# Performance work log

Hardware: AMD Instinct MI355X
Metric: run time of the kernel (lower is better)

Reference implementation:

```python
import jax, jax.numpy as jnp
import numpy as np

N, C, L, E = 10000, 128, 9, 5  # nodes, channels, (lmax+1)^2, num_elements
INV_SQRT_C = 1.0 / np.sqrt(C).astype(np.float32)


def _sparse(key, shape, p=0.15):
    # mimic the sparsity of e3nn CG coupling (U) tensors
    k1, k2 = jax.random.split(key)
    mask = jax.random.bernoulli(k1, p, shape)
    vals = jax.random.normal(k2, shape, dtype=jnp.float32)
    return jnp.where(mask, vals, 0.0)


def setup_inputs() -> dict:
    key = jax.random.key(0)
    ks = jax.random.split(key, 16)
    node_feats = jax.random.normal(ks[0], (N, C, L), dtype=jnp.float32)
    node_attrs = jax.nn.one_hot(jax.random.randint(ks[1], (N,), 0, E), E, dtype=jnp.float32)
    sc = jax.random.normal(ks[2], (N, 512), dtype=jnp.float32)
    # CG coupling tensors U_nu per output irrep (constant buffers in the torch module)
    # l_out = 0 (d=1): path counts k3=10, k2=3, k1=1
    U3_0 = _sparse(ks[3], (1, L, L, L, 10))
    U2_0 = _sparse(ks[4], (1, L, L, 3))
    U1_0 = _sparse(ks[5], (1, L, 1))
    # l_out = 1 (d=3): path counts k3=12, k2=4, k1=1
    U3_1 = _sparse(ks[6], (3, L, L, L, 12))
    U2_1 = _sparse(ks[7], (3, L, L, 4))
    U1_1 = _sparse(ks[8], (3, L, 1))
    # element-dependent contraction weights: randn(E, k, C) / k  (MACE init)
    w3_0 = jax.random.normal(ks[9], (E, 10, C), dtype=jnp.float32) / 10.0
    w2_0 = jax.random.normal(ks[10], (E, 3, C), dtype=jnp.float32) / 3.0
    w1_0 = jax.random.normal(ks[11], (E, 1, C), dtype=jnp.float32) / 1.0
    w3_1 = jax.random.normal(ks[12], (E, 12, C), dtype=jnp.float32) / 12.0
    w2_1 = jax.random.normal(ks[13], (E, 4, C), dtype=jnp.float32) / 4.0
    w1_1 = jax.random.normal(ks[14], (E, 1, C), dtype=jnp.float32) / 1.0
    # o3.Linear internal weights (one [C,C] block per output irrep)
    kl0, kl1 = jax.random.split(ks[15])
    lin_w0 = jax.random.normal(kl0, (C, C), dtype=jnp.float32)
    lin_w1 = jax.random.normal(kl1, (C, C), dtype=jnp.float32)
    return dict(node_feats=node_feats, node_attrs=node_attrs, sc=sc,
                U3_0=U3_0, U2_0=U2_0, U1_0=U1_0, w3_0=w3_0, w2_0=w2_0, w1_0=w1_0,
                U3_1=U3_1, U2_1=U2_1, U1_1=U1_1, w3_1=w3_1, w2_1=w2_1, w1_1=w1_1,
                lin_w0=lin_w0, lin_w1=lin_w1)


def _contraction(x, y, U3, U2, U1, w3, w2, w1):
    # MACE recursive symmetric contraction, correlation=3.
    # x: [N,C,L] node feats, y: [N,E] one-hot, U_nu: [d, L^nu, k_nu], w_nu: [E,k_nu,C]
    out = jnp.einsum('duvwk,ekc,bcw,be->bcduv', U3, w3, x, y)      # [N,C,d,L,L]
    c2 = jnp.einsum('duvk,ekc,be->bcduv', U2, w2, y) + out
    out = jnp.einsum('bcduv,bcv->bcdu', c2, x)                      # [N,C,d,L]
    c1 = jnp.einsum('duk,ekc,be->bcdu', U1, w1, y) + out
    out = jnp.einsum('bcdu,bcu->bcd', c1, x)                        # [N,C,d]
    return out.reshape(out.shape[0], -1)                            # [N,C*d]


def reference(node_feats, node_attrs, sc,
              U3_0, U2_0, U1_0, w3_0, w2_0, w1_0,
              U3_1, U2_1, U1_1, w3_1, w2_1, w1_1,
              lin_w0, lin_w1):
    # SymmetricContraction: one Contraction per target irrep, concat over irreps
    out0 = _contraction(node_feats, node_attrs, U3_0, U2_0, U1_0, w3_0, w2_0, w1_0)  # [N,C]
    out1 = _contraction(node_feats, node_attrs, U3_1, U2_1, U1_1, w3_1, w2_1, w1_1)  # [N,3C]
    # o3.Linear(target_irreps, target_irreps): per-l channel mixing, 1/sqrt(fan_in)
    y0 = (out0 @ lin_w0) * INV_SQRT_C                                # [N,C]
    x1 = out1.reshape(-1, C, 3)
    y1 = jnp.einsum('bcd,ce->bed', x1, lin_w1) * INV_SQRT_C          # [N,C,3]
    out = jnp.concatenate([y0, y1.reshape(-1, 3 * C)], axis=-1)      # [N,512]
    return out + sc  # use_sc residual
```

## Files before the change

### kernel.cpp

```cpp
#include <hip/hip_runtime.h>


#define CCH 128
#define LDIM 9
#define NE 5
#define BLK 256
#define TSTR 220
#define TGSTR 880
#define U3LDS 8748

__global__ __launch_bounds__(BLK) void count_offs_kernel(
    const float* __restrict__ attrs, int N,
    int* __restrict__ elem, int* __restrict__ gcnt,
    int* __restrict__ offs, int* __restrict__ cur) {
  int n = blockIdx.x * BLK + threadIdx.x;
  int e = 0;
  if (n < N) {
    const float* a = attrs + n * NE;
#pragma unroll
    for (int j = 1; j < NE; ++j)
      if (a[j] > 0.5f) e = j;
    elem[n] = e;
  }
  int lane = threadIdx.x & 63;
#pragma unroll
  for (int k = 0; k < NE; ++k) {
    unsigned long long m = __ballot(n < N && e == k);
    if (m) {
      int leader = __ffsll((long long)m) - 1;
      if (lane == leader) atomicAdd(&gcnt[k], __popcll(m));
    }
  }
  __threadfence();
  __syncthreads();
  if (threadIdx.x == 0) {
    int t = atomicAdd(&gcnt[NE], 1);
    if (t == (int)gridDim.x - 1) {
      int acc = 0;
      for (int k = 0; k < NE; ++k) {
        int ck = atomicAdd(&gcnt[k], 0);
        offs[k] = acc; cur[k] = acc; acc += ck;
      }
      offs[NE] = acc;
    }
  }
}

__global__ __launch_bounds__(BLK) void scatter_kernel(
    const int* __restrict__ elem, int N,
    int* __restrict__ cur, int* __restrict__ order) {
  int n = blockIdx.x * BLK + threadIdx.x;
  if (n >= N) return;
  int e = elem[n];
  int lane = threadIdx.x & 63;
#pragma unroll
  for (int k = 0; k < NE; ++k) {
    if (e == k) {
      unsigned long long m = __ballot(1);
      int cnt = __popcll(m);
      int leader = __ffsll((long long)m) - 1;
      int base = 0;
      if (lane == leader) base = atomicAdd(&cur[k], cnt);
      base = __shfl(base, leader);
      int rank = __popcll(m & ((1ull << lane) - 1ull));
      order[base + rank] = n;
    }
  }
}

__global__ __launch_bounds__(BLK) void table_kernel(
    const float* __restrict__ U3_0, const float* __restrict__ U2_0,
    const float* __restrict__ U1_0, const float* __restrict__ U3_1,
    const float* __restrict__ U2_1, const float* __restrict__ U1_1,
    const float* __restrict__ w3_0, const float* __restrict__ w2_0,
    const float* __restrict__ w1_0, const float* __restrict__ w3_1,
    const float* __restrict__ w2_1, const float* __restrict__ w1_1,
    float* __restrict__ table) {
  const int b = blockIdx.x;
  const int dd = blockIdx.y;
  const int e = b / CCH, c = b % CCH;
  float* Tg = table + (size_t)b * TGSTR + dd * TSTR;
  __shared__ float Us[U3LDS];
  __shared__ float U2s[324];
  __shared__ float R3[729];
  __shared__ float R2[81];
  __shared__ float R1l[9];
  __shared__ float w3l[12], w2l[4];
  const int tid = threadIdx.x;
  const int d = dd - 1;
  const int K3 = (dd == 0) ? 10 : 12;
  const int K2 = (dd == 0) ? 3 : 4;

  if (dd == 0) {
    for (int i = tid; i < 7290; i += BLK) Us[i] = U3_0[i];
    for (int i = tid; i < 243; i += BLK)  U2s[i] = U2_0[i];
    if (tid < 10) w3l[tid] = w3_0[(e * 10 + tid) * CCH + c];
    else if (tid < 13) w2l[tid - 10] = w2_0[(e * 3 + (tid - 10)) * CCH + c];
    if (tid < 9) R1l[tid] = U1_0[tid] * w1_0[e * CCH + c];
  } else {
    for (int i = tid; i < 8748; i += BLK) Us[i] = U3_1[d * 8748 + i];
    for (int i = tid; i < 324; i += BLK)  U2s[i] = U2_1[d * 324 + i];
    if (tid < 12) w3l[tid] = w3_1[(e * 12 + tid) * CCH + c];
    else if (tid < 16) w2l[tid - 12] = w2_1[(e * 4 + (tid - 12)) * CCH + c];
    if (tid < 9) R1l[tid] = U1_1[d * 9 + tid] * w1_1[e * CCH + c];
  }
  __syncthreads();
  for (int r = tid; r < 729; r += BLK) {
    float acc = 0.f;
    for (int k = 0; k < K3; ++k) acc += Us[r * K3 + k] * w3l[k];
    R3[r] = acc;
  }
  for (int q = tid; q < 81; q += BLK) {
    float acc = 0.f;
    for (int k = 0; k < K2; ++k) acc += U2s[q * K2 + k] * w2l[k];
    R2[q] = acc;
  }
  __syncthreads();
  for (int i = tid; i < TSTR; i += BLK) {
    float val = 0.f;
    if (i < 219) {
      int rem = i, u = 0;
      while (rem >= (10 - u) * (11 - u) / 2) {
        rem -= (10 - u) * (11 - u) / 2; ++u;
      }
      if (rem == 0) {
        val = R1l[u];
      } else {
        rem -= 1;
        int v = u;
        while (rem >= 10 - v) { rem -= 10 - v; ++v; }
        if (rem == 0) {
          val = (u == v) ? R2[u * 9 + v] : R2[u * 9 + v] + R2[v * 9 + u];
        } else {
          int w = v + (rem - 1);
          if (u == v && v == w)
            val = R3[(u * 9 + u) * 9 + u];
          else if (u == v)
            val = R3[(u * 9 + u) * 9 + w] + R3[(u * 9 + w) * 9 + u] +
                  R3[(w * 9 + u) * 9 + u];
          else if (v == w)
            val = R3[(u * 9 + v) * 9 + v] + R3[(v * 9 + u) * 9 + v] +
                  R3[(v * 9 + v) * 9 + u];
          else
            val = R3[(u * 9 + v) * 9 + w] + R3[(u * 9 + w) * 9 + v] +
                  R3[(v * 9 + u) * 9 + w] + R3[(v * 9 + w) * 9 + u] +
                  R3[(w * 9 + u) * 9 + v] + R3[(w * 9 + v) * 9 + u];
        }
      }
    }
    Tg[i] = val;
  }
}

__global__ __launch_bounds__(BLK, 8) void contract_kernel(
    const float* __restrict__ feats, const float* __restrict__ table,
    const int* __restrict__ order, const int* __restrict__ offs,
    float* __restrict__ tmp, int NPAD) {
  const int c = blockIdx.x;
  int rem = blockIdx.y;
  int e = -1, pbase = 0, segend = 0;
#pragma unroll
  for (int k = 0; k < NE; ++k) {
    int st = offs[k], en = offs[k + 1];
    int nc = (en - st + BLK - 1) >> 8;
    if (e < 0) {
      if (rem < nc) { e = k; pbase = st + rem * BLK; segend = en; }
      else rem -= nc;
    }
  }
  if (e < 0) return;

  const int p = pbase + threadIdx.x;
  const bool valid = (p < segend);
  const int n = order[valid ? p : (segend - 1)];

  float tf[LDIM];
  {
    const float* xp = feats + ((size_t)n * CCH + c) * LDIM;
#pragma unroll
    for (int q = 0; q < LDIM; ++q) tf[q] = xp[q];
  }

  const float* Tc = table + (size_t)(e * CCH + c) * TGSTR;

#pragma unroll 1
  for (int dd = 0; dd < 4; ++dd) {
    const float* B = Tc + dd * TSTR;
    int idx = 0;
    float acc = 0.f;
#pragma unroll
    for (int u = 0; u < 9; ++u) {
      float inner = B[idx++];
#pragma unroll
      for (int v = u; v < 9; ++v) {
        float Hv = B[idx++];
#pragma unroll
        for (int w = v; w < 9; ++w)
          Hv = fmaf(B[idx++], tf[w], Hv);
        inner = fmaf(Hv, tf[v], inner);
      }
      acc = fmaf(inner, tf[u], acc);
    }
    if (valid) tmp[((size_t)dd * CCH + c) * NPAD + p] = acc;
  }
}

#define NB 8
__global__ __launch_bounds__(BLK, 5) void linear_kernel(
    const float* __restrict__ tmp, const float* __restrict__ W0,
    const float* __restrict__ W1, const float* __restrict__ sc,
    const int* __restrict__ order, float* __restrict__ out, int N, int NPAD) {
  const int p0 = blockIdx.x * NB;
  const int t = threadIdx.x;
  __shared__ __align__(16) float SU[4128];

#pragma unroll
  for (int k = 0; k < 4; ++k) {
    int f = t + k * BLK;
    int dd = f >> 8, r = f & 255;
    int ci = r >> 1, q = r & 1;
    float4 v = *(const float4*)(tmp + (size_t)(dd * CCH + ci) * NPAD + p0 + q * 4);
    *(float4*)(SU + dd * 1024 + ci * 8 + q * 4) = v;
  }
  __syncthreads();

  const int j = t & 7;
  const int o = t >> 3;
  float acc[4][4];
#pragma unroll
  for (int dd = 0; dd < 4; ++dd)
#pragma unroll
    for (int k = 0; k < 4; ++k) acc[dd][k] = 0.f;

  const float* W0p = W0 + o * 4;
  const float* W1p = W1 + o * 4;
  float4 wa0 = *(const float4*)(W0p + 0 * CCH);
  float4 wc0 = *(const float4*)(W1p + 0 * CCH);
  float4 wa1 = *(const float4*)(W0p + 1 * CCH);
  float4 wc1 = *(const float4*)(W1p + 1 * CCH);
#pragma unroll 2
  for (int ci = 0; ci < CCH; ci += 2) {
    const int cn = (ci + 2) & 127;
    float4 pa0 = *(const float4*)(W0p + cn * CCH);
    float4 pc0 = *(const float4*)(W1p + cn * CCH);
    float4 pa1 = *(const float4*)(W0p + (cn + 1) * CCH);
    float4 pc1 = *(const float4*)(W1p + (cn + 1) * CCH);

    float a0 = SU[0 * 1024 + ci * 8 + j];
    float a1 = SU[1 * 1024 + ci * 8 + j];
    float a2 = SU[2 * 1024 + ci * 8 + j];
    float a3 = SU[3 * 1024 + ci * 8 + j];
    acc[0][0] = fmaf(a0, wa0.x, acc[0][0]);
    acc[0][1] = fmaf(a0, wa0.y, acc[0][1]);
    acc[0][2] = fmaf(a0, wa0.z, acc[0][2]);
    acc[0][3] = fmaf(a0, wa0.w, acc[0][3]);
    acc[1][0] = fmaf(a1, wc0.x, acc[1][0]);
    acc[1][1] = fmaf(a1, wc0.y, acc[1][1]);
    acc[1][2] = fmaf(a1, wc0.z, acc[1][2]);
    acc[1][3] = fmaf(a1, wc0.w, acc[1][3]);
    acc[2][0] = fmaf(a2, wc0.x, acc[2][0]);
    acc[2][1] = fmaf(a2, wc0.y, acc[2][1]);
    acc[2][2] = fmaf(a2, wc0.z, acc[2][2]);
    acc[2][3] = fmaf(a2, wc0.w, acc[2][3]);
    acc[3][0] = fmaf(a3, wc0.x, acc[3][0]);
    acc[3][1] = fmaf(a3, wc0.y, acc[3][1]);
    acc[3][2] = fmaf(a3, wc0.z, acc[3][2]);
    acc[3][3] = fmaf(a3, wc0.w, acc[3][3]);

    float b0 = SU[0 * 1024 + (ci + 1) * 8 + j];
    float b1 = SU[1 * 1024 + (ci + 1) * 8 + j];
    float b2 = SU[2 * 1024 + (ci + 1) * 8 + j];
    float b3 = SU[3 * 1024 + (ci + 1) * 8 + j];
    acc[0][0] = fmaf(b0, wa1.x, acc[0][0]);
    acc[0][1] = fmaf(b0, wa1.y, acc[0][1]);
    acc[0][2] = fmaf(b0, wa1.z, acc[0][2]);
    acc[0][3] = fmaf(b0, wa1.w, acc[0][3]);
    acc[1][0] = fmaf(b1, wc1.x, acc[1][0]);
    acc[1][1] = fmaf(b1, wc1.y, acc[1][1]);
    acc[1][2] = fmaf(b1, wc1.z, acc[1][2]);
    acc[1][3] = fmaf(b1, wc1.w, acc[1][3]);
    acc[2][0] = fmaf(b2, wc1.x, acc[2][0]);
    acc[2][1] = fmaf(b2, wc1.y, acc[2][1]);
    acc[2][2] = fmaf(b2, wc1.z, acc[2][2]);
    acc[2][3] = fmaf(b2, wc1.w, acc[2][3]);
    acc[3][0] = fmaf(b3, wc1.x, acc[3][0]);
    acc[3][1] = fmaf(b3, wc1.y, acc[3][1]);
    acc[3][2] = fmaf(b3, wc1.z, acc[3][2]);
    acc[3][3] = fmaf(b3, wc1.w, acc[3][3]);

    wa0 = pa0; wc0 = pc0; wa1 = pa1; wc1 = pc1;
  }
  __syncthreads();

  const float s = 0.08838834764831843f;
  float* Sj = SU + j * 516;
#pragma unroll
  for (int k = 0; k < 4; ++k) {
    int co = o * 4 + k;
    Sj[co]               = acc[0][k] * s;
    Sj[CCH + co * 3 + 0] = acc[1][k] * s;
    Sj[CCH + co * 3 + 1] = acc[2][k] * s;
    Sj[CCH + co * 3 + 2] = acc[3][k] * s;
  }
  __syncthreads();

  const int f = t & 127;
  const int jj = t >> 7;
#pragma unroll 1
  for (int jr = jj; jr < NB; jr += 2) {
    int p = p0 + jr;
    if (p < N) {
      int n = order[p];
      float4 sv = ((const float4*)(sc + (size_t)n * 512))[f];
      float4 ov = ((const float4*)(SU + jr * 516))[f];
      ov.x += sv.x; ov.y += sv.y; ov.z += sv.z; ov.w += sv.w;
      ((float4*)(out + (size_t)n * 512))[f] = ov;
    }
  }
}

extern "C" void kernel_launch(void* const* d_in, const int* in_sizes, int n_in,
                              void* d_out, int out_size, void* d_ws, size_t ws_size,
                              hipStream_t stream) {
  const float* feats = (const float*)d_in[0];
  const float* attrs = (const float*)d_in[1];
  const float* sc    = (const float*)d_in[2];
  const float* U3_0  = (const float*)d_in[3];
  const float* U2_0  = (const float*)d_in[4];
  const float* U1_0  = (const float*)d_in[5];
  const float* w3_0  = (const float*)d_in[6];
  const float* w2_0  = (const float*)d_in[7];
  const float* w1_0  = (const float*)d_in[8];
  const float* U3_1  = (const float*)d_in[9];
  const float* U2_1  = (const float*)d_in[10];
  const float* U1_1  = (const float*)d_in[11];
  const float* w3_1  = (const float*)d_in[12];
  const float* w2_1  = (const float*)d_in[13];
  const float* w1_1  = (const float*)d_in[14];
  const float* W0    = (const float*)d_in[15];
  const float* W1    = (const float*)d_in[16];

  const int N = in_sizes[0] / (CCH * LDIM);
  const int NPAD = ((N + 15) & ~15) + 16;

  float* table = (float*)d_ws;
  float* tmp   = table + (size_t)NE * CCH * TGSTR;
  int*   order = (int*)(tmp + (size_t)4 * CCH * NPAD);
  int*   elem  = order + N;
  int*   offs  = elem + N;
  int*   cur   = offs + 8;
  int*   gcnt  = cur + 8;
  float* out   = (float*)d_out;

  hipMemsetAsync(gcnt, 0, 8 * sizeof(int), stream);

  const int nblk = (N + BLK - 1) / BLK;
  count_offs_kernel<<<dim3(nblk), dim3(BLK), 0, stream>>>(
      attrs, N, elem, gcnt, offs, cur);
  scatter_kernel<<<dim3(nblk), dim3(BLK), 0, stream>>>(elem, N, cur, order);

  table_kernel<<<dim3(NE * CCH, 4), dim3(BLK), 0, stream>>>(
      U3_0, U2_0, U1_0, U3_1, U2_1, U1_1,
      w3_0, w2_0, w1_0, w3_1, w2_1, w1_1, table);

  const int chunksMax = (N + BLK - 1) / BLK + NE;
  contract_kernel<<<dim3(CCH, chunksMax), dim3(BLK), 0, stream>>>(
      feats, table, order, offs, tmp, NPAD);

  linear_kernel<<<dim3((N + NB - 1) / NB), dim3(BLK), 0, stream>>>(
      tmp, W0, W1, sc, order, out, N, NPAD);
}
```

Measured before the change: 266.4 us.

## Stage linear-layer weights in LDS with double-buffered async loads, 16 nodes per block

The per-node linear kernel now handles 16 nodes per block instead of 8, so each weight read serves twice as many nodes. W0/W1 are streamed into LDS in 16-row chunks with global_load_lds and double buffering, replacing per-thread global float4 loads. In exchange it uses 64KB LDS, which cuts occupancy (launch bounds drop to 2), adds a barrier per chunk, and doubles the accumulator registers. It also launches half as many blocks, which with about 625 blocks may leave compute units underused.

```diff
diff --git a/kernel.cpp b/kernel.cpp
--- a/kernel.cpp
+++ b/kernel.cpp
@@ -205,109 +205,106 @@
   }
 }
 
-#define NB 8
-__global__ __launch_bounds__(BLK, 5) void linear_kernel(
+#define NB 16
+__global__ __launch_bounds__(BLK, 2) void linear_kernel(
     const float* __restrict__ tmp, const float* __restrict__ W0,
     const float* __restrict__ W1, const float* __restrict__ sc,
     const int* __restrict__ order, float* __restrict__ out, int N, int NPAD) {
   const int p0 = blockIdx.x * NB;
   const int t = threadIdx.x;
-  __shared__ __align__(16) float SU[4128];
-
-#pragma unroll
-  for (int k = 0; k < 4; ++k) {
+  const int wave = t >> 6, lane = t & 63;
+  __shared__ __align__(16) float SU[16384];
+
+#pragma unroll
+  for (int k = 0; k < 8; ++k) {
     int f = t + k * BLK;
-    int dd = f >> 8, r = f & 255;
-    int ci = r >> 1, q = r & 1;
+    int dd = f >> 9, r = f & 511;
+    int ci = r >> 2, q = r & 3;
     float4 v = *(const float4*)(tmp + (size_t)(dd * CCH + ci) * NPAD + p0 + q * 4);
-    *(float4*)(SU + dd * 1024 + ci * 8 + q * 4) = v;
-  }
-  __syncthreads();
-
-  const int j = t & 7;
+    *(float4*)(SU + dd * 2048 + ci * 16 + q * 4) = v;
+  }
+  {
+    const int fo0 = wave * 512 + lane * 4;
+    const int fo1 = fo0 + 256;
+    __builtin_amdgcn_global_load_lds(W0 + fo0, &SU[8192 + fo0], 16, 0, 0);
+    __builtin_amdgcn_global_load_lds(W0 + fo1, &SU[8192 + fo1], 16, 0, 0);
+    __builtin_amdgcn_global_load_lds(W1 + fo0, &SU[8192 + 2048 + fo0], 16, 0, 0);
+    __builtin_amdgcn_global_load_lds(W1 + fo1, &SU[8192 + 2048 + fo1], 16, 0, 0);
+  }
+  __syncthreads();
+
+  const int j2 = t & 7;
   const int o = t >> 3;
-  float acc[4][4];
-#pragma unroll
-  for (int dd = 0; dd < 4; ++dd)
-#pragma unroll
-    for (int k = 0; k < 4; ++k) acc[dd][k] = 0.f;
-
-  const float* W0p = W0 + o * 4;
-  const float* W1p = W1 + o * 4;
-  float4 wa0 = *(const float4*)(W0p + 0 * CCH);
-  float4 wc0 = *(const float4*)(W1p + 0 * CCH);
-  float4 wa1 = *(const float4*)(W0p + 1 * CCH);
-  float4 wc1 = *(const float4*)(W1p + 1 * CCH);
-#pragma unroll 2
-  for (int ci = 0; ci < CCH; ci += 2) {
-    const int cn = (ci + 2) & 127;
-    float4 pa0 = *(const float4*)(W0p + cn * CCH);
-    float4 pc0 = *(const float4*)(W1p + cn * CCH);
-    float4 pa1 = *(const float4*)(W0p + (cn + 1) * CCH);
-    float4 pc1 = *(const float4*)(W1p + (cn + 1) * CCH);
-
-    float a0 = SU[0 * 1024 + ci * 8 + j];
-    float a1 = SU[1 * 1024 + ci * 8 + j];
-    float a2 = SU[2 * 1024 + ci * 8 + j];
-    float a3 = SU[3 * 1024 + ci * 8 + j];
-    acc[0][0] = fmaf(a0, wa0.x, acc[0][0]);
-    acc[0][1] = fmaf(a0, wa0.y, acc[0][1]);
-    acc[0][2] = fmaf(a0, wa0.z, acc[0][2]);
-    acc[0][3] = fmaf(a0, wa0.w, acc[0][3]);
-    acc[1][0] = fmaf(a1, wc0.x, acc[1][0]);
-    acc[1][1] = fmaf(a1, wc0.y, acc[1][1]);
-    acc[1][2] = fmaf(a1, wc0.z, acc[1][2]);
-    acc[1][3] = fmaf(a1, wc0.w, acc[1][3]);
-    acc[2][0] = fmaf(a2, wc0.x, acc[2][0]);
-    acc[2][1] = fmaf(a2, wc0.y, acc[2][1]);
-    acc[2][2] = fmaf(a2, wc0.z, acc[2][2]);
-    acc[2][3] = fmaf(a2, wc0.w, acc[2][3]);
-    acc[3][0] = fmaf(a3, wc0.x, acc[3][0]);
-    acc[3][1] = fmaf(a3, wc0.y, acc[3][1]);
-    acc[3][2] = fmaf(a3, wc0.z, acc[3][2]);
-    acc[3][3] = fmaf(a3, wc0.w, acc[3][3]);
-
-    float b0 = SU[0 * 1024 + (ci + 1) * 8 + j];
-    float b1 = SU[1 * 1024 + (ci + 1) * 8 + j];
-    float b2 = SU[2 * 1024 + (ci + 1) * 8 + j];
-    float b3 = SU[3 * 1024 + (ci + 1) * 8 + j];
-    acc[0][0] = fmaf(b0, wa1.x, acc[0][0]);
-    acc[0][1] = fmaf(b0, wa1.y, acc[0][1]);
-    acc[0][2] = fmaf(b0, wa1.z, acc[0][2]);
-    acc[0][3] = fmaf(b0, wa1.w, acc[0][3]);
-    acc[1][0] = fmaf(b1, wc1.x, acc[1][0]);
-    acc[1][1] = fmaf(b1, wc1.y, acc[1][1]);
-    acc[1][2] = fmaf(b1, wc1.z, acc[1][2]);
-    acc[1][3] = fmaf(b1, wc1.w, acc[1][3]);
-    acc[2][0] = fmaf(b2, wc1.x, acc[2][0]);
-    acc[2][1] = fmaf(b2, wc1.y, acc[2][1]);
-    acc[2][2] = fmaf(b2, wc1.z, acc[2][2]);
-    acc[2][3] = fmaf(b2, wc1.w, acc[2][3]);
-    acc[3][0] = fmaf(b3, wc1.x, acc[3][0]);
-    acc[3][1] = fmaf(b3, wc1.y, acc[3][1]);
-    acc[3][2] = fmaf(b3, wc1.z, acc[3][2]);
-    acc[3][3] = fmaf(b3, wc1.w, acc[3][3]);
-
-    wa0 = pa0; wc0 = pc0; wa1 = pa1; wc1 = pc1;
-  }
-  __syncthreads();
+  float acc[2][4][4];
+#pragma unroll
+  for (int jj = 0; jj < 2; ++jj)
+#pragma unroll
+    for (int dd = 0; dd < 4; ++dd)
+#pragma unroll
+      for (int k = 0; k < 4; ++k) acc[jj][dd][k] = 0.f;
+
+#pragma unroll 1
+  for (int kk = 0; kk < 8; ++kk) {
+    if (kk < 7) {
+      const int wb = 8192 + ((kk + 1) & 1) * 4096;
+      const float* s0 = W0 + (kk + 1) * 2048;
+      const float* s1 = W1 + (kk + 1) * 2048;
+      const int fo0 = wave * 512 + lane * 4;
+      const int fo1 = fo0 + 256;
+      __builtin_amdgcn_global_load_lds(s0 + fo0, &SU[wb + fo0], 16, 0, 0);
+      __builtin_amdgcn_global_load_lds(s0 + fo1, &SU[wb + fo1], 16, 0, 0);
+      __builtin_amdgcn_global_load_lds(s1 + fo0, &SU[wb + 2048 + fo0], 16, 0, 0);
+      __builtin_amdgcn_global_load_lds(s1 + fo1, &SU[wb + 2048 + fo1], 16, 0, 0);
+    }
+    const int wb = 8192 + (kk & 1) * 4096;
+#pragma unroll
+    for (int cl = 0; cl < 16; ++cl) {
+      const int ci = kk * 16 + cl;
+      const float4 wa = *(const float4*)(SU + wb + cl * 128 + o * 4);
+      const float4 wc = *(const float4*)(SU + wb + 2048 + cl * 128 + o * 4);
+      float av[4][2];
+#pragma unroll
+      for (int dd = 0; dd < 4; ++dd) {
+        av[dd][0] = SU[dd * 2048 + ci * 16 + j2];
+        av[dd][1] = SU[dd * 2048 + ci * 16 + j2 + 8];
+      }
+#pragma unroll
+      for (int jj = 0; jj < 2; ++jj) {
+        acc[jj][0][0] = fmaf(av[0][jj], wa.x, acc[jj][0][0]);
+        acc[jj][0][1] = fmaf(av[0][jj], wa.y, acc[jj][0][1]);
+        acc[jj][0][2] = fmaf(av[0][jj], wa.z, acc[jj][0][2]);
+        acc[jj][0][3] = fmaf(av[0][jj], wa.w, acc[jj][0][3]);
+#pragma unroll
+        for (int d = 1; d < 4; ++d) {
+          acc[jj][d][0] = fmaf(av[d][jj], wc.x, acc[jj][d][0]);
+          acc[jj][d][1] = fmaf(av[d][jj], wc.y, acc[jj][d][1]);
+          acc[jj][d][2] = fmaf(av[d][jj], wc.z, acc[jj][d][2]);
+          acc[jj][d][3] = fmaf(av[d][jj], wc.w, acc[jj][d][3]);
+        }
+      }
+    }
+    __syncthreads();
+  }
 
   const float s = 0.08838834764831843f;
-  float* Sj = SU + j * 516;
-#pragma unroll
-  for (int k = 0; k < 4; ++k) {
-    int co = o * 4 + k;
-    Sj[co]               = acc[0][k] * s;
-    Sj[CCH + co * 3 + 0] = acc[1][k] * s;
-    Sj[CCH + co * 3 + 1] = acc[2][k] * s;
-    Sj[CCH + co * 3 + 2] = acc[3][k] * s;
+#pragma unroll
+  for (int jj = 0; jj < 2; ++jj) {
+    float* Sj = SU + (j2 + jj * 8) * 516;
+#pragma unroll
+    for (int k = 0; k < 4; ++k) {
+      int co = o * 4 + k;
+      Sj[co]               = acc[jj][0][k] * s;
+      Sj[CCH + co * 3 + 0] = acc[jj][1][k] * s;
+      Sj[CCH + co * 3 + 1] = acc[jj][2][k] * s;
+      Sj[CCH + co * 3 + 2] = acc[jj][3][k] * s;
+    }
   }
   __syncthreads();
 
   const int f = t & 127;
-  const int jj = t >> 7;
+  const int jj4 = t >> 7;
 #pragma unroll 1
-  for (int jr = jj; jr < NB; jr += 2) {
+  for (int jr = jj4; jr < NB; jr += 2) {
     int p = p0 + jr;
     if (p < N) {
       int n = order[p];
```

Result: faster. 259.5 us (-2.6%).
